# Kernel optimization log

Hardware: AMD Instinct MI355X
Metric: run time of the kernel (lower is better)

The kernel has to match this reference:

```python
import jax, jax.numpy as jnp
import numpy as np

B, T, CH, V, E, L = 64, 1024, 256, 32000, 64, 128  # batch, enc_len, channel, vocab, emb_dim, latent_dims


def setup_inputs() -> dict:
    key = jax.random.key(0)
    ks = jax.random.split(key, 13)
    s = 0.05  # weight init scale
    return {
        "prev_cont_vec": jax.random.normal(ks[0], (B, CH), jnp.float32),
        "F": jax.random.normal(ks[1], (B, T, CH), jnp.float32),
        "prev_char": jax.random.normal(ks[2], (B, V), jnp.float32),
        "state_h": jax.random.normal(ks[3], (B, L), jnp.float32),
        "state_c": jax.random.normal(ks[4], (B, L), jnp.float32),
        # learned parameters (all Dense layers use_bias=False)
        "Wc": jax.random.normal(ks[5], (V, E), jnp.float32) * s,
        "Wct1": jax.random.normal(ks[6], (CH, E), jnp.float32) * s,
        "Wo": jax.random.normal(ks[7], (L, V), jnp.float32) * s,
        "Wct2": jax.random.normal(ks[8], (CH, V), jnp.float32) * s,
        "lstm_kernel": jax.random.normal(ks[9], (E, 4 * L), jnp.float32) * s,
        "lstm_recurrent": jax.random.normal(ks[10], (L, 4 * L), jnp.float32) * s,
        "W_h": jax.random.normal(ks[11], (L, CH), jnp.float32) * s,
        "V_attn": jax.random.normal(ks[12], (1, 1, CH), jnp.float32) * s,
    }


def reference(prev_cont_vec, F, prev_char, state_h, state_c,
              Wc, Wct1, Wo, Wct2, lstm_kernel, lstm_recurrent, W_h, V_attn):
    # lstm input: Wc(prev_char) + Wct1(prev_cont_vec)  -> [B, E]
    lstm_inp = prev_char @ Wc + prev_cont_vec @ Wct1
    # Keras LSTMCell (no bias), gate order i, f, c, o
    z = lstm_inp @ lstm_kernel + state_h @ lstm_recurrent  # [B, 4L]
    zi, zf, zg, zo = jnp.split(z, 4, axis=-1)
    i = jax.nn.sigmoid(zi)
    f = jax.nn.sigmoid(zf)
    g = jnp.tanh(zg)
    o = jax.nn.sigmoid(zo)
    new_c = f * state_c + i * g
    new_h = o * jnp.tanh(new_c)
    # training=True branch: clip returned cell state
    new_c_out = jnp.clip(new_c, -10.0, 10.0)
    # additive attention over time axis of F [B, T, CH]
    H_tfm = (new_h @ W_h)[:, None, :]            # [B, 1, CH]
    e_t = V_attn * jnp.tanh(H_tfm + F)           # [B, T, CH]
    attn = jax.nn.softmax(e_t, axis=1)           # softmax over T, per channel
    c_t = jnp.sum(attn * F, axis=1)              # [B, CH]
    # output distribution
    O_t = jax.nn.softmax(new_h @ Wo + c_t @ Wct2, axis=1)  # [B, V]
    return (O_t, c_t, new_h, new_c_out)
```

## Files before the change

kernel.cpp:

```cpp
#include <hip/hip_runtime.h>
#include <hip/hip_bf16.h>

#define BB 64
#define TT 1024
#define CHN 256
#define VV 32000
#define EE 64
#define LL 128
#define NC1 250
#define KC1 128
#define TS 16

typedef unsigned short u16;
typedef unsigned int u32;
typedef __attribute__((ext_vector_type(8))) short short8;
typedef __attribute__((ext_vector_type(16))) float f32x16;

__device__ __forceinline__ float fast_rcp(float x) { return __builtin_amdgcn_rcpf(x); }
__device__ __forceinline__ float tanh_fast(float y) {
    float e = __expf(2.0f * y);
    return 1.0f - 2.0f * fast_rcp(1.0f + e);
}
__device__ __forceinline__ float sigmoid_fast(float x) {
    return fast_rcp(1.0f + __expf(-x));
}
__device__ __forceinline__ u16 f2bf(float f) {
    u32 u = __float_as_uint(f);
    return (u16)((u + 0x7fffu + ((u >> 16) & 1u)) >> 16);
}
__device__ __forceinline__ u32 pack_bf2(float lo, float hi) {
    return (u32)f2bf(lo) | ((u32)f2bf(hi) << 16);
}

__global__ __launch_bounds__(256) void k1_stage1(const float* __restrict__ A,
                                                 const float* __restrict__ Wc,
                                                 float* __restrict__ part) {
    __shared__ float sW[KC1][EE];
    __shared__ float sAT[KC1][32];
    const int kc = blockIdx.x;
    const int k0 = kc * KC1;
    const int y  = blockIdx.y;
    const int t  = threadIdx.x;

    #pragma unroll
    for (int f = t; f < 2048; f += 256)
        *(float4*)(&sW[0][0] + f * 4) = *(const float4*)(Wc + (size_t)k0 * EE + f * 4);
    {
        const int bl = t & 31;
        const int kq = t >> 5;
        const float* src = A + (size_t)(y * 32 + bl) * VV + k0 + kq * 16;
        #pragma unroll
        for (int j4 = 0; j4 < 4; ++j4) {
            float4 v = *(const float4*)(src + j4 * 4);
            sAT[kq * 16 + j4 * 4 + 0][bl] = v.x;
            sAT[kq * 16 + j4 * 4 + 1][bl] = v.y;
            sAT[kq * 16 + j4 * 4 + 2][bl] = v.z;
            sAT[kq * 16 + j4 * 4 + 3][bl] = v.w;
        }
    }
    __syncthreads();

    const int e  = t & 63;
    const int b0 = (t >> 6) * 8;
    float acc[8];
    #pragma unroll
    for (int i = 0; i < 8; ++i) acc[i] = 0.0f;

    #pragma unroll 4
    for (int k = 0; k < KC1; ++k) {
        float wt = sW[k][e];
        float4 a0 = *(const float4*)&sAT[k][b0];
        float4 a1 = *(const float4*)&sAT[k][b0 + 4];
        acc[0] = fmaf(a0.x, wt, acc[0]);
        acc[1] = fmaf(a0.y, wt, acc[1]);
        acc[2] = fmaf(a0.z, wt, acc[2]);
        acc[3] = fmaf(a0.w, wt, acc[3]);
        acc[4] = fmaf(a1.x, wt, acc[4]);
        acc[5] = fmaf(a1.y, wt, acc[5]);
        acc[6] = fmaf(a1.z, wt, acc[6]);
        acc[7] = fmaf(a1.w, wt, acc[7]);
    }
    const int gb = y * 32 + b0;
    #pragma unroll
    for (int i = 0; i < 8; ++i)
        part[((size_t)(gb + i) * NC1 + kc) * EE + e] = acc[i];
}

__global__ __launch_bounds__(512) void k2_lstm(const float* __restrict__ part,
    const float* __restrict__ pcv, const float* __restrict__ state_h,
    const float* __restrict__ state_c, const float* __restrict__ Wct1,
    const float* __restrict__ lstm_kernel, const float* __restrict__ lstm_rec,
    const float* __restrict__ W_h,
    float* __restrict__ out_newh, float* __restrict__ out_newc,
    u32* __restrict__ Apk, float* __restrict__ Htfm) {
    __shared__ float red[8][EE];
    __shared__ float inp[EE];
    __shared__ float sh[LL];
    __shared__ float z[4 * LL];
    __shared__ float nh[LL];
    const int b = blockIdx.x;
    const int t = threadIdx.x;
    const int e  = t & 63;
    const int g  = t >> 6;

    {
        float s = 0.0f;
        for (int j = g; j < NC1; j += 8)
            s += part[((size_t)b * NC1 + j) * EE + e];
        const int c0 = g * 32;
        #pragma unroll 8
        for (int c = 0; c < 32; ++c)
            s = fmaf(pcv[b * CHN + c0 + c], Wct1[(size_t)(c0 + c) * EE + e], s);
        red[g][e] = s;
    }
    __syncthreads();
    if (t < EE) {
        float s = 0.0f;
        #pragma unroll
        for (int j = 0; j < 8; ++j) s += red[j][t];
        inp[t] = s;
    } else if (t >= 64 && t < 64 + LL) {
        sh[t - 64] = state_h[b * LL + (t - 64)];
    }
    __syncthreads();
    {
        float a = 0.0f;
        #pragma unroll 8
        for (int e2 = 0; e2 < EE; ++e2) a = fmaf(inp[e2], lstm_kernel[e2 * 512 + t], a);
        #pragma unroll 8
        for (int l = 0; l < LL; ++l) a = fmaf(sh[l], lstm_rec[l * 512 + t], a);
        z[t] = a;
    }
    __syncthreads();
    if (t < LL) {
        float zi = z[t], zf = z[LL + t], zg = z[2 * LL + t], zo = z[3 * LL + t];
        float ig = sigmoid_fast(zi);
        float fg = sigmoid_fast(zf);
        float gg = tanh_fast(zg);
        float og = sigmoid_fast(zo);
        float co = state_c[b * LL + t];
        float cn = fg * co + ig * gg;
        float hn = og * tanh_fast(cn);
        out_newc[b * LL + t] = fminf(fmaxf(cn, -10.0f), 10.0f);
        out_newh[b * LL + t] = hn;
        nh[t] = hn;
    }
    __syncthreads();
    if (t < CHN) {
        float a = 0.0f;
        #pragma unroll 8
        for (int l = 0; l < LL; ++l) a = fmaf(nh[l], W_h[l * CHN + t], a);
        Htfm[b * CHN + t] = a;
    } else if (t >= CHN && t < CHN + 64) {
        const int k2i = t - CHN;
        Apk[(size_t)k2i * BB + b] = pack_bf2(nh[2 * k2i], nh[2 * k2i + 1]);
    }
}

__global__ __launch_bounds__(256) void k3_attn(const float* __restrict__ F,
    const float* __restrict__ Htfm, const float* __restrict__ Vattn,
    float* __restrict__ pS, float* __restrict__ pW) {
    __shared__ float4 sS[256];
    __shared__ float4 sW[256];
    const int b    = blockIdx.x;
    const int ts   = blockIdx.y;
    const int lane = threadIdx.x & 63;
    const int w    = threadIdx.x >> 6;
    const int ch   = lane * 4;

    float4 h = *(const float4*)(Htfm + b * CHN + ch);
    float4 v = *(const float4*)(Vattn + ch);
    float s0 = 0, s1 = 0, s2 = 0, s3 = 0;
    float a0 = 0, a1 = 0, a2 = 0, a3 = 0;

    const float* Fp = F + ((size_t)b * TT + ts * (TT / TS) + w * 16) * CHN + ch;
    float4 cur = *(const float4*)(Fp);
    #pragma unroll
    for (int t = 0; t < 16; ++t) {
        float4 nxt;
        if (t < 15) nxt = *(const float4*)(Fp + (size_t)(t + 1) * CHN);
        float e0 = __expf(v.x * tanh_fast(h.x + cur.x));
        float e1 = __expf(v.y * tanh_fast(h.y + cur.y));
        float e2 = __expf(v.z * tanh_fast(h.z + cur.z));
        float e3 = __expf(v.w * tanh_fast(h.w + cur.w));
        s0 += e0; s1 += e1; s2 += e2; s3 += e3;
        a0 = fmaf(e0, cur.x, a0); a1 = fmaf(e1, cur.y, a1);
        a2 = fmaf(e2, cur.z, a2); a3 = fmaf(e3, cur.w, a3);
        cur = nxt;
    }
    sS[threadIdx.x] = make_float4(s0, s1, s2, s3);
    sW[threadIdx.x] = make_float4(a0, a1, a2, a3);
    __syncthreads();
    if (threadIdx.x < 64) {
        float4 S = sS[threadIdx.x];
        float4 W = sW[threadIdx.x];
        #pragma unroll
        for (int j = 1; j < 4; ++j) {
            float4 s = sS[j * 64 + threadIdx.x];
            float4 q = sW[j * 64 + threadIdx.x];
            S.x += s.x; S.y += s.y; S.z += s.z; S.w += s.w;
            W.x += q.x; W.y += q.y; W.z += q.z; W.w += q.w;
        }
        int base = (b * TS + ts) * CHN + threadIdx.x * 4;
        *(float4*)(pS + base) = S;
        *(float4*)(pW + base) = W;
    }
}

__global__ __launch_bounds__(256) void k4_combine(const float* __restrict__ pS,
    const float* __restrict__ pW, float* __restrict__ out_ct, u32* __restrict__ Apk) {
    __shared__ float sc[CHN];
    const int b = blockIdx.x;
    const int ch = threadIdx.x;
    float S = 0.0f, W = 0.0f;
    #pragma unroll
    for (int j = 0; j < TS; ++j) {
        int idx = (b * TS + j) * CHN + ch;
        S += pS[idx];
        W += pW[idx];
    }
    float c = W / S;
    out_ct[b * CHN + ch] = c;
    sc[ch] = c;
    __syncthreads();
    if (ch < 128)
        Apk[(size_t)(64 + ch) * BB + b] = pack_bf2(sc[2 * ch], sc[2 * ch + 1]);
}

__global__ __launch_bounds__(256) void k5_logits(const float* __restrict__ Wo,
    const float* __restrict__ Wct2, const u32* __restrict__ Apk,
    float* __restrict__ outO, float* __restrict__ psum) {
    __shared__ float rp[4][32];
    const int t    = threadIdx.x;
    const int lane = t & 63;
    const int wv   = t >> 6;
    const int m    = lane & 31;
    const int kq   = lane >> 5;
    const int y    = blockIdx.y;
    const int n0   = blockIdx.x * 128 + wv * 32;
    const int gb0  = y * 32;

    u32 af[24][4];
    #pragma unroll
    for (int tt = 0; tt < 24; ++tt) {
        #pragma unroll
        for (int r = 0; r < 4; ++r)
            af[tt][r] = Apk[(size_t)(tt * 8 + kq * 4 + r) * BB + gb0 + m];
    }

    f32x16 acc = {0.0f, 0.0f, 0.0f, 0.0f, 0.0f, 0.0f, 0.0f, 0.0f,
                  0.0f, 0.0f, 0.0f, 0.0f, 0.0f, 0.0f, 0.0f, 0.0f};

    float wbuf[2][8];
    {
        const float* c0 = Wo + (size_t)(kq * 8) * VV + n0 + m;
        #pragma unroll
        for (int j = 0; j < 8; ++j) wbuf[0][j] = c0[(size_t)j * VV];
    }

    #pragma unroll
    for (int tt = 0; tt < 24; ++tt) {
        if (tt < 23) {
            const int kn = (tt + 1) * 16 + kq * 8;
            const float* cn = (kn < LL ? Wo + (size_t)kn * VV
                                       : Wct2 + (size_t)(kn - LL) * VV) + n0 + m;
            #pragma unroll
            for (int j = 0; j < 8; ++j) wbuf[(tt + 1) & 1][j] = cn[(size_t)j * VV];
        }
        short8 a, b;
        #pragma unroll
        for (int r = 0; r < 4; ++r) {
            u32 lo = __float_as_uint(wbuf[tt & 1][2 * r]);
            u32 hi = __float_as_uint(wbuf[tt & 1][2 * r + 1]);
            u32 bp = (lo >> 16) | (hi & 0xffff0000u);
            u32 ap = af[tt][r];
            a[2 * r]     = (short)(ap & 0xffff);
            a[2 * r + 1] = (short)(ap >> 16);
            b[2 * r]     = (short)(bp & 0xffff);
            b[2 * r + 1] = (short)(bp >> 16);
        }
        acc = __builtin_amdgcn_mfma_f32_32x32x16_bf16(a, b, acc, 0, 0, 0);
    }

    float ex[16];
    #pragma unroll
    for (int r = 0; r < 16; ++r) {
        const int row = (r & 3) + 8 * (r >> 2) + 4 * kq;
        ex[r] = __expf(acc[r]);
        outO[(size_t)(gb0 + row) * VV + n0 + m] = ex[r];
    }
    #pragma unroll
    for (int r = 0; r < 16; ++r) {
        float s = ex[r];
        s += __shfl_xor(s, 1, 64);  s += __shfl_xor(s, 2, 64);
        s += __shfl_xor(s, 4, 64);  s += __shfl_xor(s, 8, 64);
        s += __shfl_xor(s, 16, 64);
        ex[r] = s;
    }
    if (m == 0) {
        #pragma unroll
        for (int r = 0; r < 16; ++r)
            rp[wv][(r & 3) + 8 * (r >> 2) + 4 * kq] = ex[r];
    }
    __syncthreads();
    if (t < 32)
        psum[(size_t)blockIdx.x * BB + gb0 + t] =
            rp[0][t] + rp[1][t] + rp[2][t] + rp[3][t];
}

__global__ __launch_bounds__(256) void k5b_rowsum(const float* __restrict__ psum,
                                                  float* __restrict__ rowsum) {
    __shared__ float red[256];
    const int t = threadIdx.x;
    const int b = t & 63;
    const int q = t >> 6;
    float s = 0.0f;
    for (int x = q; x < NC1; x += 4) s += psum[x * BB + b];
    red[t] = s;
    __syncthreads();
    if (t < 64) rowsum[b] = red[b] + red[64 + b] + red[128 + b] + red[192 + b];
}

__global__ __launch_bounds__(256) void k5c_norm(float* __restrict__ O,
                                                const float* __restrict__ rowsum) {
    const int gid = blockIdx.x * 256 + threadIdx.x;
    float4* O4 = (float4*)O;
    const u32 row = ((u32)gid * 4u) / (u32)VV;
    const float inv = fast_rcp(rowsum[row]);
    float4 f = O4[gid];
    f.x *= inv; f.y *= inv; f.z *= inv; f.w *= inv;
    O4[gid] = f;
}

extern "C" void kernel_launch(void* const* d_in, const int* in_sizes, int n_in,
                              void* d_out, int out_size, void* d_ws, size_t ws_size,
                              hipStream_t stream) {
    (void)in_sizes; (void)n_in; (void)out_size; (void)ws_size;
    const float* pcv       = (const float*)d_in[0];
    const float* F         = (const float*)d_in[1];
    const float* prev_char = (const float*)d_in[2];
    const float* state_h   = (const float*)d_in[3];
    const float* state_c   = (const float*)d_in[4];
    const float* Wc        = (const float*)d_in[5];
    const float* Wct1      = (const float*)d_in[6];
    const float* Wo        = (const float*)d_in[7];
    const float* Wct2      = (const float*)d_in[8];
    const float* lstm_k    = (const float*)d_in[9];
    const float* lstm_r    = (const float*)d_in[10];
    const float* W_h       = (const float*)d_in[11];
    const float* Vattn     = (const float*)d_in[12];

    float* outO  = (float*)d_out;
    float* outCt = outO + (size_t)BB * VV;
    float* outH  = outCt + (size_t)BB * CHN;
    float* outC  = outH + (size_t)BB * LL;

    float* ws     = (float*)d_ws;
    float* part   = ws;
    float* pS     = part + (size_t)NC1 * BB * EE;
    float* pW     = pS + (size_t)BB * TS * CHN;
    float* Htfm   = pW + (size_t)BB * TS * CHN;
    float* psum   = Htfm + (size_t)BB * CHN;
    float* rowsum = psum + (size_t)NC1 * BB;
    u32*   Apk    = (u32*)(rowsum + BB);

    hipLaunchKernelGGL(k1_stage1, dim3(NC1, 2), dim3(256), 0, stream, prev_char, Wc, part);
    hipLaunchKernelGGL(k2_lstm, dim3(BB), dim3(512), 0, stream, part, pcv, state_h,
                       state_c, Wct1, lstm_k, lstm_r, W_h, outH, outC, Apk, Htfm);
    hipLaunchKernelGGL(k3_attn, dim3(BB, TS), dim3(256), 0, stream, F, Htfm, Vattn, pS, pW);
    hipLaunchKernelGGL(k4_combine, dim3(BB), dim3(256), 0, stream, pS, pW, outCt, Apk);
    hipLaunchKernelGGL(k5_logits, dim3(NC1, 2), dim3(256), 0, stream, Wo, Wct2, Apk, outO, psum);
    hipLaunchKernelGGL(k5b_rowsum, dim3(1), dim3(256), 0, stream, psum, rowsum);
    hipLaunchKernelGGL(k5c_norm, dim3((BB * VV / 4) / 256), dim3(256), 0, stream, outO, rowsum);
}
```

Before: 233.7 us.

## Store unnormalized exps as bf16 and fuse rowsum into normalization kernel

The logits kernel now writes exp values as bf16 into workspace instead of fp32 into the output, and a single normalization kernel reduces the per-block partial sums, then reads the bf16 values and writes the normalized fp32 output. This halves the intermediate traffic for the 64x32000 tensor and removes the single-block rowsum launch. The packed activation matrix is also re-laid out so each lane loads a uint4 instead of four scalar loads. Rounding exps to bf16 adds precision error to the softmax output.

```diff
diff --git a/kernel.cpp b/kernel.cpp
--- a/kernel.cpp
+++ b/kernel.cpp
@@ -30,6 +30,12 @@
 }
 __device__ __forceinline__ u32 pack_bf2(float lo, float hi) {
     return (u32)f2bf(lo) | ((u32)f2bf(hi) << 16);
+}
+__device__ __forceinline__ float bf2f(u16 x) {
+    return __uint_as_float(((u32)x) << 16);
+}
+__device__ __forceinline__ size_t apk_idx(int g, int b) {
+    return ((size_t)(((g >> 3) * 2 + ((g & 7) >> 2)) * 64 + b)) * 4 + (g & 3);
 }
 
 __global__ __launch_bounds__(256) void k1_stage1(const float* __restrict__ A,
@@ -105,6 +111,7 @@
 
     {
         float s = 0.0f;
+        #pragma unroll 4
         for (int j = g; j < NC1; j += 8)
             s += part[((size_t)b * NC1 + j) * EE + e];
         const int c0 = g * 32;
@@ -152,8 +159,8 @@
         for (int l = 0; l < LL; ++l) a = fmaf(nh[l], W_h[l * CHN + t], a);
         Htfm[b * CHN + t] = a;
     } else if (t >= CHN && t < CHN + 64) {
-        const int k2i = t - CHN;
-        Apk[(size_t)k2i * BB + b] = pack_bf2(nh[2 * k2i], nh[2 * k2i + 1]);
+        const int gp = t - CHN;
+        Apk[apk_idx(gp, b)] = pack_bf2(nh[2 * gp], nh[2 * gp + 1]);
     }
 }
 
@@ -224,12 +231,12 @@
     sc[ch] = c;
     __syncthreads();
     if (ch < 128)
-        Apk[(size_t)(64 + ch) * BB + b] = pack_bf2(sc[2 * ch], sc[2 * ch + 1]);
+        Apk[apk_idx(64 + ch, b)] = pack_bf2(sc[2 * ch], sc[2 * ch + 1]);
 }
 
 __global__ __launch_bounds__(256) void k5_logits(const float* __restrict__ Wo,
     const float* __restrict__ Wct2, const u32* __restrict__ Apk,
-    float* __restrict__ outO, float* __restrict__ psum) {
+    u16* __restrict__ expb, float* __restrict__ psum) {
     __shared__ float rp[4][32];
     const int t    = threadIdx.x;
     const int lane = t & 63;
@@ -240,13 +247,10 @@
     const int n0   = blockIdx.x * 128 + wv * 32;
     const int gb0  = y * 32;
 
-    u32 af[24][4];
-    #pragma unroll
-    for (int tt = 0; tt < 24; ++tt) {
-        #pragma unroll
-        for (int r = 0; r < 4; ++r)
-            af[tt][r] = Apk[(size_t)(tt * 8 + kq * 4 + r) * BB + gb0 + m];
-    }
+    uint4 af[24];
+    #pragma unroll
+    for (int tt = 0; tt < 24; ++tt)
+        af[tt] = *(const uint4*)&Apk[((size_t)((tt * 2 + kq) * 64) + gb0 + m) * 4];
 
     f32x16 acc = {0.0f, 0.0f, 0.0f, 0.0f, 0.0f, 0.0f, 0.0f, 0.0f,
                   0.0f, 0.0f, 0.0f, 0.0f, 0.0f, 0.0f, 0.0f, 0.0f};
@@ -268,12 +272,13 @@
             for (int j = 0; j < 8; ++j) wbuf[(tt + 1) & 1][j] = cn[(size_t)j * VV];
         }
         short8 a, b;
+        u32 ax = af[tt].x, ay = af[tt].y, az = af[tt].z, aw = af[tt].w;
         #pragma unroll
         for (int r = 0; r < 4; ++r) {
             u32 lo = __float_as_uint(wbuf[tt & 1][2 * r]);
             u32 hi = __float_as_uint(wbuf[tt & 1][2 * r + 1]);
             u32 bp = (lo >> 16) | (hi & 0xffff0000u);
-            u32 ap = af[tt][r];
+            u32 ap = (r == 0) ? ax : (r == 1) ? ay : (r == 2) ? az : aw;
             a[2 * r]     = (short)(ap & 0xffff);
             a[2 * r + 1] = (short)(ap >> 16);
             b[2 * r]     = (short)(bp & 0xffff);
@@ -287,7 +292,7 @@
     for (int r = 0; r < 16; ++r) {
         const int row = (r & 3) + 8 * (r >> 2) + 4 * kq;
         ex[r] = __expf(acc[r]);
-        outO[(size_t)(gb0 + row) * VV + n0 + m] = ex[r];
+        expb[(size_t)(gb0 + row) * VV + n0 + m] = f2bf(ex[r]);
     }
     #pragma unroll
     for (int r = 0; r < 16; ++r) {
@@ -308,28 +313,34 @@
             rp[0][t] + rp[1][t] + rp[2][t] + rp[3][t];
 }
 
-__global__ __launch_bounds__(256) void k5b_rowsum(const float* __restrict__ psum,
-                                                  float* __restrict__ rowsum) {
+__global__ __launch_bounds__(256) void k5c_norm(const u16* __restrict__ expb,
+    const float* __restrict__ psum, float* __restrict__ O) {
     __shared__ float red[256];
-    const int t = threadIdx.x;
-    const int b = t & 63;
-    const int q = t >> 6;
-    float s = 0.0f;
-    for (int x = q; x < NC1; x += 4) s += psum[x * BB + b];
-    red[t] = s;
-    __syncthreads();
-    if (t < 64) rowsum[b] = red[b] + red[64 + b] + red[128 + b] + red[192 + b];
-}
-
-__global__ __launch_bounds__(256) void k5c_norm(float* __restrict__ O,
-                                                const float* __restrict__ rowsum) {
-    const int gid = blockIdx.x * 256 + threadIdx.x;
-    float4* O4 = (float4*)O;
-    const u32 row = ((u32)gid * 4u) / (u32)VV;
-    const float inv = fast_rcp(rowsum[row]);
-    float4 f = O4[gid];
-    f.x *= inv; f.y *= inv; f.z *= inv; f.w *= inv;
-    O4[gid] = f;
+    const int b   = blockIdx.x;
+    const int seg = blockIdx.y;
+    const int t   = threadIdx.x;
+
+    red[t] = (t < NC1) ? psum[(size_t)t * BB + b] : 0.0f;
+    __syncthreads();
+    #pragma unroll
+    for (int off = 128; off > 0; off >>= 1) {
+        if (t < off) red[t] += red[t + off];
+        __syncthreads();
+    }
+    const float inv = fast_rcp(red[0]);
+
+    const u16* src = expb + (size_t)b * VV + seg * 8000;
+    float* dst     = O + (size_t)b * VV + seg * 8000;
+    #pragma unroll 2
+    for (int i = t; i < 2000; i += 256) {
+        uint2 pk = *(const uint2*)(src + i * 4);
+        float4 f;
+        f.x = bf2f((u16)(pk.x & 0xffff)) * inv;
+        f.y = bf2f((u16)(pk.x >> 16)) * inv;
+        f.z = bf2f((u16)(pk.y & 0xffff)) * inv;
+        f.w = bf2f((u16)(pk.y >> 16)) * inv;
+        *(float4*)(dst + i * 4) = f;
+    }
 }
 
 extern "C" void kernel_launch(void* const* d_in, const int* in_sizes, int n_in,
@@ -361,15 +372,14 @@
     float* pW     = pS + (size_t)BB * TS * CHN;
     float* Htfm   = pW + (size_t)BB * TS * CHN;
     float* psum   = Htfm + (size_t)BB * CHN;
-    float* rowsum = psum + (size_t)NC1 * BB;
-    u32*   Apk    = (u32*)(rowsum + BB);
+    u32*   Apk    = (u32*)(psum + (size_t)NC1 * BB);
+    u16*   expb   = (u16*)(Apk + 12288);
 
     hipLaunchKernelGGL(k1_stage1, dim3(NC1, 2), dim3(256), 0, stream, prev_char, Wc, part);
     hipLaunchKernelGGL(k2_lstm, dim3(BB), dim3(512), 0, stream, part, pcv, state_h,
                        state_c, Wct1, lstm_k, lstm_r, W_h, outH, outC, Apk, Htfm);
     hipLaunchKernelGGL(k3_attn, dim3(BB, TS), dim3(256), 0, stream, F, Htfm, Vattn, pS, pW);
     hipLaunchKernelGGL(k4_combine, dim3(BB), dim3(256), 0, stream, pS, pW, outCt, Apk);
-    hipLaunchKernelGGL(k5_logits, dim3(NC1, 2), dim3(256), 0, stream, Wo, Wct2, Apk, outO, psum);
-    hipLaunchKernelGGL(k5b_rowsum, dim3(1), dim3(256), 0, stream, psum, rowsum);
-    hipLaunchKernelGGL(k5c_norm, dim3((BB * VV / 4) / 256), dim3(256), 0, stream, outO, rowsum);
-}
+    hipLaunchKernelGGL(k5_logits, dim3(NC1, 2), dim3(256), 0, stream, Wo, Wct2, Apk, expb, psum);
+    hipLaunchKernelGGL(k5c_norm, dim3(BB, 4), dim3(256), 0, stream, expb, psum, outO);
+}
```

Result: faster. 221.4 us (-5.3%).
